# Kernel tuning notes

Hardware: AMD Instinct MI355X
Metric: run time of the kernel (lower is better)

Reference implementation:

```python
import jax, jax.numpy as jnp
import numpy as np

N, IN_F, OUT_F, HID, R = 384, 64, 4, 32, 16
EPS = 1e-5
CUT_LO, CUT_HI = 0.0, 5.0


def _expnormal_smearing(dist):
    # dist: [N, N, 1] -> [N, N, R]; torchmd-net ExpNormalSmearing with cosine cutoff
    alpha = 5.0 / (CUT_HI - CUT_LO)
    start = float(np.exp(-CUT_HI + CUT_LO))
    means = jnp.linspace(start, 1.0, R, dtype=dist.dtype)          # [R]
    beta = (2.0 / R * (1.0 - start)) ** -2
    cutoff = 0.5 * (jnp.cos(dist * jnp.pi / CUT_HI) + 1.0) * (dist < CUT_HI)
    return cutoff * jnp.exp(-beta * (jnp.exp(alpha * (CUT_LO - dist)) - means) ** 2)


def setup_inputs() -> dict:
    key = jax.random.key(0)
    k = jax.random.split(key, 5)
    x = jax.random.normal(k[0], (N, 3), dtype=jnp.float32) * 2.0        # node positions
    h = jax.random.normal(k[1], (N, IN_F), dtype=jnp.float32)           # node features
    W_fc = jax.random.normal(k[2], (2 * R * HID, IN_F), dtype=jnp.float32) / np.sqrt(IN_F)
    W_sum = jax.random.normal(k[3], (2 * OUT_F * R, HID), dtype=jnp.float32) / np.sqrt(HID)
    b_sum = jnp.zeros((2 * OUT_F * R,), dtype=jnp.float32)
    return {"x": x, "h": h, "W_fc": W_fc, "W_sum": W_sum, "b_sum": b_sum}


def reference(x, h, W_fc, W_sum, b_sum):
    # --- TransductiveParameter.forward ---
    hp = h @ W_fc.T                                  # [N, 2*R*H]
    hp = hp[:, None, :] + hp[None, :, :]             # [N, N, 2*R*H]
    K, Q = jnp.split(hp, 2, axis=-1)                 # each [N, N, R*H]
    K = K.reshape(N, N, R, HID)
    Q = Q.reshape(N, N, R, HID)

    # --- JunmaiLayer.forward ---
    dx = x[:, None, :] - x[None, :, :]               # [N, N, 3]
    nsq = jnp.sum(dx * dx, axis=-1, keepdims=True) + EPS
    nrm = jnp.sqrt(nsq)                              # [N, N, 1]
    dxn = dx / nsq                                   # [N, N, 3]
    smear = _expnormal_smearing(nrm)                 # [N, N, R]
    basis = smear[..., None] * dxn[..., None, :]     # [N, N, R, 3]

    bk = jnp.einsum('mnrb,mnrc->mcb', basis, K)      # [N, H, 3]
    bq = jnp.einsum('mnrb,mnrc->mcb', basis, Q)      # [N, H, 3]
    att = jnp.sum(bk * bq, axis=-1)                  # [N, H]
    out = jax.nn.silu(att) @ W_sum.T + b_sum         # [N, 2*out*R]

    hh = out.reshape(N, R, 2 * OUT_F)
    hh = hh[:, None, :, :] + hh[None, :, :, :]       # [N, N, R, 2*out]
    K2, Q2 = jnp.split(hh, 2, axis=-1)               # each [N, N, R, out]
    return (K2, Q2)
```

## Files before the change

### kernel.cpp

```cpp
#include <hip/hip_runtime.h>
#include <math.h>

#define NN 384
#define IN_F 64
#define HID 32
#define RR 16
#define HP_W 1024
#define EPSF 1e-5f
#define CHUNK 48
#define NCHUNK 8
#define MT 2

typedef float f4 __attribute__((ext_vector_type(4)));

__global__ __launch_bounds__(256) void k_hp(const float* __restrict__ h,
                                            const float* __restrict__ Wfc,
                                            float* __restrict__ hpT) {
    int m = blockIdx.x;
    int tid = threadIdx.x;
    __shared__ float4 hs4[IN_F / 4];
    if (tid < IN_F / 4) hs4[tid] = ((const float4*)(h + m * IN_F))[tid];
    __syncthreads();
    const float4* W4 = (const float4*)Wfc;
    for (int jj = 0; jj < 4; ++jj) {
        int j = tid + 256 * jj;
        const float4* row = W4 + (size_t)j * (IN_F / 4);
        float acc = 0.f;
#pragma unroll
        for (int k = 0; k < IN_F / 4; ++k) {
            float4 w = row[k];
            float4 hv = hs4[k];
            acc += w.x * hv.x + w.y * hv.y + w.z * hv.z + w.w * hv.w;
        }
        int kq = j >> 9, rc = j & 511, r = rc >> 5, c = rc & 31;
        hpT[(size_t)m * HP_W + kq * 512 + c * 16 + r] = acc;
    }
}

__global__ __launch_bounds__(256) void k_mid(const float* __restrict__ x,
                                             const float* __restrict__ hpT,
                                             float* __restrict__ pbk,
                                             float* __restrict__ pS,
                                             float beta, float start) {
    const int ch = blockIdx.x;
    const int m0 = blockIdx.y * MT;
    const int n0 = ch * CHUNK;
    const int tid = threadIdx.x;

    __shared__ float smear_s[MT][CHUNK][16];
    __shared__ float dxn_s[MT][CHUNK][3];
    __shared__ float red_s[4][MT][64][3];

    for (int it = tid; it < MT * CHUNK * 16; it += 256) {
        int mi = it / (CHUNK * 16);
        int rest = it % (CHUNK * 16);
        int np = rest >> 4, r = rest & 15;
        int m = m0 + mi, n = n0 + np;
        float d0 = x[m * 3 + 0] - x[n * 3 + 0];
        float d1 = x[m * 3 + 1] - x[n * 3 + 1];
        float d2 = x[m * 3 + 2] - x[n * 3 + 2];
        float nsq = d0 * d0 + d1 * d1 + d2 * d2 + EPSF;
        float dist = sqrtf(nsq);
        float cut = (dist < 5.0f) ? 0.5f * (__cosf(dist * 0.62831853071795864769f) + 1.0f) : 0.0f;
        float en = __expf(-dist);
        float mean_r = start + (1.0f - start) * ((float)r * (1.0f / 15.0f));
        float dmr = en - mean_r;
        smear_s[mi][np][r] = cut * __expf(-beta * dmr * dmr);
        if (r < 3) dxn_s[mi][np][r] = ((r == 0) ? d0 : ((r == 1) ? d1 : d2)) / nsq;
    }
    __syncthreads();

    const int g = tid >> 6, kq = (tid >> 5) & 1, c = tid & 31;
    float a00 = 0.f, a01 = 0.f, a02 = 0.f, a10 = 0.f, a11 = 0.f, a12 = 0.f;
    const float* hpbase = hpT + (size_t)(n0 + g * 12) * HP_W + kq * 512 + c * 16;
    for (int ni = 0; ni < 12; ++ni) {
        const int np = g * 12 + ni;
        const float4* hp4 = (const float4*)(hpbase + (size_t)ni * HP_W);
        float4 h0 = hp4[0], h1 = hp4[1], h2 = hp4[2], h3 = hp4[3];
        {
            const float4* sm4 = (const float4*)smear_s[0][np];
            float4 s0 = sm4[0], s1 = sm4[1], s2 = sm4[2], s3 = sm4[3];
            float P = h0.x * s0.x + h0.y * s0.y + h0.z * s0.z + h0.w * s0.w
                    + h1.x * s1.x + h1.y * s1.y + h1.z * s1.z + h1.w * s1.w
                    + h2.x * s2.x + h2.y * s2.y + h2.z * s2.z + h2.w * s2.w
                    + h3.x * s3.x + h3.y * s3.y + h3.z * s3.z + h3.w * s3.w;
            a00 += P * dxn_s[0][np][0];
            a01 += P * dxn_s[0][np][1];
            a02 += P * dxn_s[0][np][2];
        }
        {
            const float4* sm4 = (const float4*)smear_s[1][np];
            float4 s0 = sm4[0], s1 = sm4[1], s2 = sm4[2], s3 = sm4[3];
            float P = h0.x * s0.x + h0.y * s0.y + h0.z * s0.z + h0.w * s0.w
                    + h1.x * s1.x + h1.y * s1.y + h1.z * s1.z + h1.w * s1.w
                    + h2.x * s2.x + h2.y * s2.y + h2.z * s2.z + h2.w * s2.w
                    + h3.x * s3.x + h3.y * s3.y + h3.z * s3.z + h3.w * s3.w;
            a10 += P * dxn_s[1][np][0];
            a11 += P * dxn_s[1][np][1];
            a12 += P * dxn_s[1][np][2];
        }
    }
    red_s[g][0][kq * 32 + c][0] = a00;
    red_s[g][0][kq * 32 + c][1] = a01;
    red_s[g][0][kq * 32 + c][2] = a02;
    red_s[g][1][kq * 32 + c][0] = a10;
    red_s[g][1][kq * 32 + c][1] = a11;
    red_s[g][1][kq * 32 + c][2] = a12;

    float accS = 0.f;
    int smi = 0, ss = 0;
    if (tid < MT * 48) {
        smi = tid / 48; ss = tid % 48;
        const int r = ss / 3, b = ss % 3;
        for (int np = 0; np < CHUNK; ++np)
            accS += smear_s[smi][np][r] * dxn_s[smi][np][b];
    }
    __syncthreads();

    for (int it = tid; it < MT * 192; it += 256) {
        int mi = it / 192, j = it % 192;
        int kq2 = j / 96, b2 = (j % 96) / 32, c2 = j % 32;
        float v = red_s[0][mi][kq2 * 32 + c2][b2] + red_s[1][mi][kq2 * 32 + c2][b2]
                + red_s[2][mi][kq2 * 32 + c2][b2] + red_s[3][mi][kq2 * 32 + c2][b2];
        pbk[((size_t)(m0 + mi) * NCHUNK + ch) * 192 + j] = v;
    }
    if (tid < MT * 48)
        pS[((size_t)(m0 + smi) * NCHUNK + ch) * 48 + ss] = accS;
}

__global__ __launch_bounds__(256) void k_combine(const float* __restrict__ hpT,
                                                 const float* __restrict__ Wsum,
                                                 const float* __restrict__ bsum,
                                                 const float* __restrict__ pbk,
                                                 const float* __restrict__ pS,
                                                 float* __restrict__ outv) {
    const int m = blockIdx.x;
    const int tid = threadIdx.x;
    __shared__ float S_s[16][3];
    __shared__ float bkq_s[2][HID][3];
    __shared__ float silu_s[HID];

    float v = 0.f;
    if (tid < 192) {
        for (int chn = 0; chn < NCHUNK; ++chn)
            v += pbk[((size_t)m * NCHUNK + chn) * 192 + tid];
    } else if (tid < 240) {
        int s = tid - 192;
        float a = 0.f;
        for (int chn = 0; chn < NCHUNK; ++chn)
            a += pS[((size_t)m * NCHUNK + chn) * 48 + s];
        S_s[s / 3][s % 3] = a;
    }
    __syncthreads();
    if (tid < 192) {
        const int kq = tid / 96, b = (tid % 96) / 32, cc = tid % 32;
        const float4* hb = (const float4*)(hpT + (size_t)m * HP_W + kq * 512 + cc * 16);
        float4 h0 = hb[0], h1 = hb[1], h2 = hb[2], h3 = hb[3];
        v += h0.x * S_s[0][b] + h0.y * S_s[1][b] + h0.z * S_s[2][b] + h0.w * S_s[3][b]
           + h1.x * S_s[4][b] + h1.y * S_s[5][b] + h1.z * S_s[6][b] + h1.w * S_s[7][b]
           + h2.x * S_s[8][b] + h2.y * S_s[9][b] + h2.z * S_s[10][b] + h2.w * S_s[11][b]
           + h3.x * S_s[12][b] + h3.y * S_s[13][b] + h3.z * S_s[14][b] + h3.w * S_s[15][b];
        bkq_s[kq][cc][b] = v;
    }
    __syncthreads();
    if (tid < HID) {
        float a = bkq_s[0][tid][0] * bkq_s[1][tid][0]
                + bkq_s[0][tid][1] * bkq_s[1][tid][1]
                + bkq_s[0][tid][2] * bkq_s[1][tid][2];
        silu_s[tid] = a / (1.0f + __expf(-a));
    }
    __syncthreads();
    if (tid < 128) {
        float acc = bsum[tid];
        const float* wr = Wsum + tid * HID;
#pragma unroll
        for (int c2 = 0; c2 < HID; ++c2) acc += wr[c2] * silu_s[c2];
        outv[(size_t)m * 128 + tid] = acc;
    }
}

__global__ __launch_bounds__(256) void k_expand(const float* __restrict__ outv,
                                                float* __restrict__ out) {
    const int bid = blockIdx.x;
    const int m = bid / 24;
    const int n0 = (bid % 24) * 16;
    const int tid = threadIdx.x;
    __shared__ float4 om[32];
    if (tid < 32) om[tid] = ((const float4*)(outv + (size_t)m * 128))[tid];
    __syncthreads();
    const int ni = tid >> 4;
    const int r = tid & 15;
    const int n = n0 + ni;
    const float4* on = (const float4*)(outv + (size_t)n * 128);
    float4 a0 = om[2 * r], a1 = om[2 * r + 1];
    float4 b0 = on[2 * r], b1 = on[2 * r + 1];
    f4 k2 = {a0.x + b0.x, a0.y + b0.y, a0.z + b0.z, a0.w + b0.w};
    f4 q2 = {a1.x + b1.x, a1.y + b1.y, a1.z + b1.z, a1.w + b1.w};
    f4* o4 = (f4*)out;
    const size_t idx = ((size_t)(m * NN + n) * RR + r);
    __builtin_nontemporal_store(k2, o4 + idx);
    __builtin_nontemporal_store(q2, o4 + (size_t)NN * NN * RR + idx);
}

extern "C" void kernel_launch(void* const* d_in, const int* in_sizes, int n_in,
                              void* d_out, int out_size, void* d_ws, size_t ws_size,
                              hipStream_t stream) {
    const float* x    = (const float*)d_in[0];
    const float* h    = (const float*)d_in[1];
    const float* Wfc  = (const float*)d_in[2];
    const float* Wsum = (const float*)d_in[3];
    const float* bsum = (const float*)d_in[4];
    float* out = (float*)d_out;

    float* hpT  = (float*)d_ws;
    float* pbk  = hpT + (size_t)NN * HP_W;
    float* pS   = pbk + (size_t)NN * NCHUNK * 192;
    float* outv = pS + (size_t)NN * NCHUNK * 48;

    double startd = exp(-5.0);
    double rd = (2.0 / 16.0) * (1.0 - startd);
    float beta = (float)(1.0 / (rd * rd));
    float start = (float)startd;

    k_hp<<<NN, 256, 0, stream>>>(h, Wfc, hpT);
    k_mid<<<dim3(NCHUNK, NN / MT), 256, 0, stream>>>(x, hpT, pbk, pS, beta, start);
    k_combine<<<NN, 256, 0, stream>>>(hpT, Wsum, bsum, pbk, pS, outv);
    k_expand<<<NN * 24, 256, 0, stream>>>(outv, out);
}
```

Baseline: 68.74 us.

## Fuse four kernel launches into one cooperative kernel with grid syncs

Replaces the four-kernel pipeline with a single cooperative persistent kernel that runs each stage in a grid-stride loop and separates the stages with grid.sync(). The aim is to remove launch gaps and tail effects between the small kernels. In exchange it adds grid-wide barrier cost and a grid size tied to an assumed 256 CUs. It also calls an occupancy query on every invocation and falls back to the old launches if the cooperative launch fails.

Result: slower. 223.4 us (+225.0%).

```diff
diff --git a/kernel.cpp b/kernel.cpp
--- a/kernel.cpp
+++ b/kernel.cpp
@@ -1,5 +1,8 @@
 #include <hip/hip_runtime.h>
+#include <hip/hip_cooperative_groups.h>
 #include <math.h>
+
+namespace cg = cooperative_groups;
 
 #define NN 384
 #define IN_F 64
@@ -10,8 +13,196 @@
 #define CHUNK 48
 #define NCHUNK 8
 #define MT 2
+#define VB_TOTAL 1536
 
 typedef float f4 __attribute__((ext_vector_type(4)));
+
+__global__ __launch_bounds__(256) void k_fused(const float* __restrict__ x,
+                                               const float* __restrict__ h,
+                                               const float* __restrict__ Wfc,
+                                               const float* __restrict__ Wsum,
+                                               const float* __restrict__ bsum,
+                                               float* __restrict__ hpT,
+                                               float* __restrict__ pbk,
+                                               float* __restrict__ pS,
+                                               float* __restrict__ outv,
+                                               float* __restrict__ out,
+                                               float beta, float start) {
+    cg::grid_group grid = cg::this_grid();
+    const int tid = threadIdx.x;
+
+    __shared__ float smear_s[MT][CHUNK][16];
+    __shared__ float dxn_s[MT][CHUNK][3];
+    __shared__ float red_s[4][MT][64][3];
+    __shared__ float S_s[16][3];
+    __shared__ float bkq_s[2][HID][3];
+    __shared__ float silu_s[HID];
+    __shared__ float4 om[32];
+
+    for (int vb = blockIdx.x; vb < NN * 4; vb += gridDim.x) {
+        const int m = vb >> 2, q = vb & 3;
+        const int j = q * 256 + tid;
+        const float4* hrow = (const float4*)(h + m * IN_F);
+        const float4* row = (const float4*)Wfc + (size_t)j * (IN_F / 4);
+        float acc = 0.f;
+#pragma unroll
+        for (int k = 0; k < IN_F / 4; ++k) {
+            float4 w = row[k];
+            float4 hv = hrow[k];
+            acc += w.x * hv.x + w.y * hv.y + w.z * hv.z + w.w * hv.w;
+        }
+        const int kq = j >> 9, rc = j & 511, r = rc >> 5, c = rc & 31;
+        hpT[(size_t)m * HP_W + kq * 512 + c * 16 + r] = acc;
+    }
+    grid.sync();
+
+    for (int vb = blockIdx.x; vb < VB_TOTAL; vb += gridDim.x) {
+        const int ch = vb & 7;
+        const int m0 = (vb >> 3) * MT;
+        const int n0 = ch * CHUNK;
+
+        for (int it = tid; it < MT * CHUNK * 16; it += 256) {
+            int mi = it / (CHUNK * 16);
+            int rest = it % (CHUNK * 16);
+            int np = rest >> 4, r = rest & 15;
+            int m = m0 + mi, n = n0 + np;
+            float d0 = x[m * 3 + 0] - x[n * 3 + 0];
+            float d1 = x[m * 3 + 1] - x[n * 3 + 1];
+            float d2 = x[m * 3 + 2] - x[n * 3 + 2];
+            float nsq = d0 * d0 + d1 * d1 + d2 * d2 + EPSF;
+            float dist = sqrtf(nsq);
+            float cut = (dist < 5.0f) ? 0.5f * (__cosf(dist * 0.62831853071795864769f) + 1.0f) : 0.0f;
+            float en = __expf(-dist);
+            float mean_r = start + (1.0f - start) * ((float)r * (1.0f / 15.0f));
+            float dmr = en - mean_r;
+            smear_s[mi][np][r] = cut * __expf(-beta * dmr * dmr);
+            if (r < 3) dxn_s[mi][np][r] = ((r == 0) ? d0 : ((r == 1) ? d1 : d2)) / nsq;
+        }
+        __syncthreads();
+
+        const int g = tid >> 6, kq = (tid >> 5) & 1, c = tid & 31;
+        float a00 = 0.f, a01 = 0.f, a02 = 0.f, a10 = 0.f, a11 = 0.f, a12 = 0.f;
+        const float* hpbase = hpT + (size_t)(n0 + g * 12) * HP_W + kq * 512 + c * 16;
+        for (int ni = 0; ni < 12; ++ni) {
+            const int np = g * 12 + ni;
+            const float4* hp4 = (const float4*)(hpbase + (size_t)ni * HP_W);
+            float4 h0 = hp4[0], h1 = hp4[1], h2 = hp4[2], h3 = hp4[3];
+            {
+                const float4* sm4 = (const float4*)smear_s[0][np];
+                float4 s0 = sm4[0], s1 = sm4[1], s2 = sm4[2], s3 = sm4[3];
+                float P = h0.x * s0.x + h0.y * s0.y + h0.z * s0.z + h0.w * s0.w
+                        + h1.x * s1.x + h1.y * s1.y + h1.z * s1.z + h1.w * s1.w
+                        + h2.x * s2.x + h2.y * s2.y + h2.z * s2.z + h2.w * s2.w
+                        + h3.x * s3.x + h3.y * s3.y + h3.z * s3.z + h3.w * s3.w;
+                a00 += P * dxn_s[0][np][0];
+                a01 += P * dxn_s[0][np][1];
+                a02 += P * dxn_s[0][np][2];
+            }
+            {
+                const float4* sm4 = (const float4*)smear_s[1][np];
+                float4 s0 = sm4[0], s1 = sm4[1], s2 = sm4[2], s3 = sm4[3];
+                float P = h0.x * s0.x + h0.y * s0.y + h0.z * s0.z + h0.w * s0.w
+                        + h1.x * s1.x + h1.y * s1.y + h1.z * s1.z + h1.w * s1.w
+                        + h2.x * s2.x + h2.y * s2.y + h2.z * s2.z + h2.w * s2.w
+                        + h3.x * s3.x + h3.y * s3.y + h3.z * s3.z + h3.w * s3.w;
+                a10 += P * dxn_s[1][np][0];
+                a11 += P * dxn_s[1][np][1];
+                a12 += P * dxn_s[1][np][2];
+            }
+        }
+        red_s[g][0][kq * 32 + c][0] = a00;
+        red_s[g][0][kq * 32 + c][1] = a01;
+        red_s[g][0][kq * 32 + c][2] = a02;
+        red_s[g][1][kq * 32 + c][0] = a10;
+        red_s[g][1][kq * 32 + c][1] = a11;
+        red_s[g][1][kq * 32 + c][2] = a12;
+
+        float accS = 0.f;
+        int smi = 0, ss = 0;
+        if (tid < MT * 48) {
+            smi = tid / 48; ss = tid % 48;
+            const int r = ss / 3, bb = ss % 3;
+            for (int np = 0; np < CHUNK; ++np)
+                accS += smear_s[smi][np][r] * dxn_s[smi][np][bb];
+        }
+        __syncthreads();
+
+        for (int it = tid; it < MT * 192; it += 256) {
+            int mi = it / 192, j = it % 192;
+            int kq2 = j / 96, b2 = (j % 96) / 32, c2 = j % 32;
+            float v = red_s[0][mi][kq2 * 32 + c2][b2] + red_s[1][mi][kq2 * 32 + c2][b2]
+                    + red_s[2][mi][kq2 * 32 + c2][b2] + red_s[3][mi][kq2 * 32 + c2][b2];
+            pbk[((size_t)(m0 + mi) * NCHUNK + ch) * 192 + j] = v;
+        }
+        if (tid < MT * 48)
+            pS[((size_t)(m0 + smi) * NCHUNK + ch) * 48 + ss] = accS;
+    }
+    grid.sync();
+
+    for (int vb = blockIdx.x; vb < NN; vb += gridDim.x) {
+        const int m = vb;
+        float v = 0.f;
+        if (tid < 192) {
+            for (int chn = 0; chn < NCHUNK; ++chn)
+                v += pbk[((size_t)m * NCHUNK + chn) * 192 + tid];
+        } else if (tid < 240) {
+            int s = tid - 192;
+            float a = 0.f;
+            for (int chn = 0; chn < NCHUNK; ++chn)
+                a += pS[((size_t)m * NCHUNK + chn) * 48 + s];
+            S_s[s / 3][s % 3] = a;
+        }
+        __syncthreads();
+        if (tid < 192) {
+            const int kq = tid / 96, bb = (tid % 96) / 32, cc = tid % 32;
+            const float4* hb = (const float4*)(hpT + (size_t)m * HP_W + kq * 512 + cc * 16);
+            float4 h0 = hb[0], h1 = hb[1], h2 = hb[2], h3 = hb[3];
+            v += h0.x * S_s[0][bb] + h0.y * S_s[1][bb] + h0.z * S_s[2][bb] + h0.w * S_s[3][bb]
+               + h1.x * S_s[4][bb] + h1.y * S_s[5][bb] + h1.z * S_s[6][bb] + h1.w * S_s[7][bb]
+               + h2.x * S_s[8][bb] + h2.y * S_s[9][bb] + h2.z * S_s[10][bb] + h2.w * S_s[11][bb]
+               + h3.x * S_s[12][bb] + h3.y * S_s[13][bb] + h3.z * S_s[14][bb] + h3.w * S_s[15][bb];
+            bkq_s[kq][cc][bb] = v;
+        }
+        __syncthreads();
+        if (tid < HID) {
+            float a = bkq_s[0][tid][0] * bkq_s[1][tid][0]
+                    + bkq_s[0][tid][1] * bkq_s[1][tid][1]
+                    + bkq_s[0][tid][2] * bkq_s[1][tid][2];
+            silu_s[tid] = a / (1.0f + __expf(-a));
+        }
+        __syncthreads();
+        if (tid < 128) {
+            float acc = bsum[tid];
+            const float* wr = Wsum + tid * HID;
+#pragma unroll
+            for (int c2 = 0; c2 < HID; ++c2) acc += wr[c2] * silu_s[c2];
+            outv[(size_t)m * 128 + tid] = acc;
+        }
+        __syncthreads();
+    }
+    grid.sync();
+
+    for (int vb = blockIdx.x; vb < NN * 4; vb += gridDim.x) {
+        const int m = vb >> 2;
+        if (tid < 32) om[tid] = ((const float4*)(outv + (size_t)m * 128))[tid];
+        __syncthreads();
+        const int ni = tid >> 4, r = tid & 15;
+        const float4 a0 = om[2 * r], a1 = om[2 * r + 1];
+        f4* o4 = (f4*)out;
+#pragma unroll
+        for (int i = 0; i < 6; ++i) {
+            const int n = ((vb & 3) * 6 + i) * 16 + ni;
+            const float4* on = (const float4*)(outv + (size_t)n * 128);
+            float4 b0 = on[2 * r], b1 = on[2 * r + 1];
+            f4 k2 = {a0.x + b0.x, a0.y + b0.y, a0.z + b0.z, a0.w + b0.w};
+            f4 q2 = {a1.x + b1.x, a1.y + b1.y, a1.z + b1.z, a1.w + b1.w};
+            const size_t idx = ((size_t)(m * NN + n) * RR + r);
+            __builtin_nontemporal_store(k2, o4 + idx);
+            __builtin_nontemporal_store(q2, o4 + (size_t)NN * NN * RR + idx);
+        }
+        __syncthreads();
+    }
+}
 
 __global__ __launch_bounds__(256) void k_hp(const float* __restrict__ h,
                                             const float* __restrict__ Wfc,
@@ -222,8 +413,24 @@
     float beta = (float)(1.0 / (rd * rd));
     float start = (float)startd;
 
-    k_hp<<<NN, 256, 0, stream>>>(h, Wfc, hpT);
-    k_mid<<<dim3(NCHUNK, NN / MT), 256, 0, stream>>>(x, hpT, pbk, pS, beta, start);
-    k_combine<<<NN, 256, 0, stream>>>(hpT, Wsum, bsum, pbk, pS, outv);
-    k_expand<<<NN * 24, 256, 0, stream>>>(outv, out);
-}
+    bool coop_ok = false;
+    int occ = 0;
+    hipError_t oerr = hipOccupancyMaxActiveBlocksPerMultiprocessor(&occ, k_fused, 256, 0);
+    if (oerr == hipSuccess && occ > 0) {
+        int gridN = occ * 256;
+        if (gridN > VB_TOTAL) gridN = VB_TOTAL;
+        void* args[] = {(void*)&x, (void*)&h, (void*)&Wfc, (void*)&Wsum, (void*)&bsum,
+                        (void*)&hpT, (void*)&pbk, (void*)&pS, (void*)&outv, (void*)&out,
+                        (void*)&beta, (void*)&start};
+        hipError_t lerr = hipLaunchCooperativeKernel((const void*)k_fused, dim3(gridN),
+                                                     dim3(256), args, 0, stream);
+        coop_ok = (lerr == hipSuccess);
+    }
+
+    if (!coop_ok) {
+        k_hp<<<NN, 256, 0, stream>>>(h, Wfc, hpT);
+        k_mid<<<dim3(NCHUNK, NN / MT), 256, 0, stream>>>(x, hpT, pbk, pS, beta, start);
+        k_combine<<<NN, 256, 0, stream>>>(hpT, Wsum, bsum, pbk, pS, outv);
+        k_expand<<<NN * 24, 256, 0, stream>>>(outv, out);
+    }
+}
```
